# Kernel optimization log

Hardware: AMD Instinct MI355X
Metric: run time of the kernel (lower is better)

## Reference

```python
import jax, jax.numpy as jnp
import numpy as np

B, S, H, V = 256, 15, 512, 50257

def setup_inputs() -> dict:
    key = jax.random.key(0)
    ks = jax.random.split(key, 12)
    sc_h = 1.0 / np.sqrt(H)
    sc_in = 1.0 / np.sqrt(2 * H)
    return {
        "input_tokens": jax.random.randint(ks[0], (B, 1), 0, V),
        "hidden": jax.random.normal(ks[1], (1, B, H), jnp.float32),
        "encoder_outputs": jax.random.normal(ks[2], (B, S, H), jnp.float32),
        "emb_table": jax.random.normal(ks[3], (V, H), jnp.float32),
        "attn_W": jax.random.uniform(ks[4], (H, H), jnp.float32, -sc_h, sc_h),
        "attn_b": jax.random.uniform(ks[5], (H,), jnp.float32, -sc_h, sc_h),
        "W_ih": jax.random.uniform(ks[6], (3 * H, 2 * H), jnp.float32, -sc_in, sc_in),
        "W_hh": jax.random.uniform(ks[7], (3 * H, H), jnp.float32, -sc_h, sc_h),
        "b_ih": jax.random.uniform(ks[8], (3 * H,), jnp.float32, -sc_h, sc_h),
        "b_hh": jax.random.uniform(ks[9], (3 * H,), jnp.float32, -sc_h, sc_h),
        "out_W": jax.random.uniform(ks[10], (V, H), jnp.float32, -sc_h, sc_h),
        "out_b": jax.random.uniform(ks[11], (V,), jnp.float32, -sc_h, sc_h),
    }


def reference(input_tokens, hidden, encoder_outputs, emb_table, attn_W, attn_b,
              W_ih, W_hh, b_ih, b_hh, out_W, out_b):
    # Embedding (dropout is identity in eval/reference mode): [B,1,H]
    embedded = emb_table[input_tokens]
    h = hidden[0]  # [B,H]

    # Bahdanau-style scores, vectorized over the seq dim instead of the python loop:
    # energies[b,s] = attn(enc[b,s]);  score[b,s] = <h[b], energies[b,s]>
    energies = jnp.einsum("bsh,oh->bso", encoder_outputs, attn_W) + attn_b  # [B,S,H]
    attn_scores = jnp.einsum("bso,bo->bs", energies, h)                      # [B,S]
    attn_weights = jax.nn.softmax(attn_scores, axis=1)                       # [B,S]

    # context = weights @ encoder_outputs: [B,1,H]
    context = jnp.einsum("bs,bsh->bh", attn_weights, encoder_outputs)[:, None, :]

    # GRU single step (PyTorch gate order: r, z, n)
    x = jnp.concatenate([embedded, context], axis=2)[:, 0]  # [B,2H]
    gi = x @ W_ih.T + b_ih   # [B,3H]
    gh = h @ W_hh.T + b_hh   # [B,3H]
    i_r, i_z, i_n = jnp.split(gi, 3, axis=1)
    h_r, h_z, h_n = jnp.split(gh, 3, axis=1)
    r = jax.nn.sigmoid(i_r + h_r)
    z = jax.nn.sigmoid(i_z + h_z)
    n = jnp.tanh(i_n + r * h_n)
    h_new = (1.0 - z) * n + z * h            # [B,H]

    logits = h_new[:, None, :] @ out_W.T + out_b   # [B,1,V]
    log_probs = jax.nn.log_softmax(logits, axis=-1)
    return log_probs, h_new[None], attn_weights
```

## Files before the change

kernel.cpp:

```cpp
#include <hip/hip_runtime.h>

#define V_SIZE 50257
#define B_SIZE 256
#define S_LEN  15
#define H_DIM  512
#define NBLK_LG 1571

typedef __attribute__((ext_vector_type(8))) short bf16x8;
typedef __attribute__((ext_vector_type(4))) float f32x4;

__device__ __forceinline__ unsigned short f2bf(float f) {
    unsigned int u = __float_as_uint(f);
    u += 0x7fffu + ((u >> 16) & 1u);
    return (unsigned short)(u >> 16);
}

__global__ __launch_bounds__(256) void u_kernel(
    const float* __restrict__ hidden, const float* __restrict__ attn_W,
    float* __restrict__ u)
{
    __shared__ float h_s[16][H_DIM];
    const int tid = threadIdx.x;
    const int b0 = blockIdx.y * 16, n0 = blockIdx.x * 32;
    const float4* hv = (const float4*)(hidden + (size_t)b0 * H_DIM);
    float4* hs4 = (float4*)&h_s[0][0];
    #pragma unroll
    for (int i = 0; i < 8; ++i) hs4[tid + i * 256] = hv[tid + i * 256];
    __syncthreads();
    const int n = n0 + (tid & 31);
    const int m = (tid >> 5) * 2;
    float a0 = 0.f, a1 = 0.f;
    #pragma unroll 8
    for (int o = 0; o < H_DIM; ++o) {
        float w = attn_W[(size_t)o * H_DIM + n];
        a0 += h_s[m][o] * w;
        a1 += h_s[m + 1][o] * w;
    }
    u[(size_t)(b0 + m) * H_DIM + n] = a0;
    u[(size_t)(b0 + m + 1) * H_DIM + n] = a1;
}

__global__ __launch_bounds__(256) void attn_kernel(
    const float* __restrict__ hidden, const float* __restrict__ enc,
    const float* __restrict__ u, const int* __restrict__ tokens,
    const float* __restrict__ emb, float* __restrict__ attnw_out,
    unsigned short* __restrict__ x_bf, unsigned short* __restrict__ h_bf)
{
    const int b = blockIdx.x, tid = threadIdx.x;
    __shared__ float u_s[H_DIM];
    __shared__ float sc_s[S_LEN];
    __shared__ float w_s[S_LEN];
    u_s[tid]       = u[(size_t)b * H_DIM + tid];
    u_s[tid + 256] = u[(size_t)b * H_DIM + tid + 256];
    h_bf[(size_t)b * H_DIM + tid]       = f2bf(hidden[(size_t)b * H_DIM + tid]);
    h_bf[(size_t)b * H_DIM + tid + 256] = f2bf(hidden[(size_t)b * H_DIM + tid + 256]);
    const int tok = tokens[b];
    x_bf[(size_t)b * 2 * H_DIM + tid]       = f2bf(emb[(size_t)tok * H_DIM + tid]);
    x_bf[(size_t)b * 2 * H_DIM + tid + 256] = f2bf(emb[(size_t)tok * H_DIM + tid + 256]);
    __syncthreads();
    const int wave = tid >> 6, lane = tid & 63;
    for (int s = wave; s < S_LEN; s += 4) {
        const float* e = enc + ((size_t)b * S_LEN + s) * H_DIM;
        float acc = 0.f;
        #pragma unroll
        for (int k = 0; k < H_DIM / 64; ++k) acc += e[lane + k * 64] * u_s[lane + k * 64];
        #pragma unroll
        for (int off = 32; off; off >>= 1) acc += __shfl_down(acc, off);
        if (lane == 0) sc_s[s] = acc;
    }
    __syncthreads();
    float mx = -1e30f;
    for (int s = 0; s < S_LEN; ++s) mx = fmaxf(mx, sc_s[s]);
    float sum = 0.f;
    for (int s = 0; s < S_LEN; ++s) sum += __expf(sc_s[s] - mx);
    const float inv = 1.f / sum;
    if (tid < S_LEN) {
        float w = __expf(sc_s[tid] - mx) * inv;
        w_s[tid] = w;
        attnw_out[b * S_LEN + tid] = w;
    }
    __syncthreads();
    #pragma unroll
    for (int hh = 0; hh < 2; ++hh) {
        int h = tid + hh * 256;
        float c = 0.f;
        #pragma unroll
        for (int s = 0; s < S_LEN; ++s)
            c += w_s[s] * enc[((size_t)b * S_LEN + s) * H_DIM + h];
        x_bf[(size_t)b * 2 * H_DIM + H_DIM + h] = f2bf(c);
    }
}

struct GemmP {
    const unsigned short* A; const float* B; const float* bias; float* C;
    int N; int K;
};

template<int BM, int BN, int BK, int WR, int WC>
__global__ __launch_bounds__(256) void gemm_nt(GemmP p0, GemmP p1)
{
    GemmP p = (blockIdx.z == 0) ? p0 : p1;
    constexpr int LDA = BK + 8;
    __shared__ __align__(16) unsigned short As[BM][LDA];
    __shared__ __align__(16) unsigned short Bs[BN][LDA];
    const int tid = threadIdx.x;
    const int bn0 = blockIdx.x * BN;
    const int bm0 = blockIdx.y * BM;
    const int wave = tid >> 6, lane = tid & 63;
    const int wm = (wave / WC) * (BM / WR);
    const int wn = (wave % WC) * (BN / WC);
    constexpr int MF = BM / WR / 16, NF = BN / WC / 16;
    const int n16 = lane & 15, quad = lane >> 4;

    f32x4 acc[MF][NF] = {};

    for (int k0 = 0; k0 < p.K; k0 += BK) {
        #pragma unroll
        for (int it = 0; it < BM / 32; ++it) {
            int v = it * 256 + tid;
            int row = v >> 3, seg = v & 7;
            *(uint4*)&As[row][seg * 8] =
                *(const uint4*)(p.A + (size_t)(bm0 + row) * p.K + k0 + seg * 8);
        }
        #pragma unroll
        for (int it = 0; it < BN / 32; ++it) {
            int v = it * 256 + tid;
            int row = v >> 3, seg = v & 7;
            int gv = bn0 + row;
            float4 w0 = make_float4(0, 0, 0, 0), w1 = make_float4(0, 0, 0, 0);
            if (gv < p.N) {
                const float4* src = (const float4*)(p.B + (size_t)gv * p.K + k0 + seg * 8);
                w0 = src[0]; w1 = src[1];
            }
            uint4 pk;
            pk.x = (unsigned)f2bf(w0.x) | ((unsigned)f2bf(w0.y) << 16);
            pk.y = (unsigned)f2bf(w0.z) | ((unsigned)f2bf(w0.w) << 16);
            pk.z = (unsigned)f2bf(w1.x) | ((unsigned)f2bf(w1.y) << 16);
            pk.w = (unsigned)f2bf(w1.z) | ((unsigned)f2bf(w1.w) << 16);
            *(uint4*)&Bs[row][seg * 8] = pk;
        }
        __syncthreads();
        #pragma unroll
        for (int kk = 0; kk < BK; kk += 32) {
            bf16x8 af[MF], bfr[NF];
            #pragma unroll
            for (int i = 0; i < MF; ++i)
                af[i] = *(const bf16x8*)&As[wm + i * 16 + n16][kk + quad * 8];
            #pragma unroll
            for (int j = 0; j < NF; ++j)
                bfr[j] = *(const bf16x8*)&Bs[wn + j * 16 + n16][kk + quad * 8];
            #pragma unroll
            for (int i = 0; i < MF; ++i)
                #pragma unroll
                for (int j = 0; j < NF; ++j)
                    acc[i][j] = __builtin_amdgcn_mfma_f32_16x16x32_bf16(
                        af[i], bfr[j], acc[i][j], 0, 0, 0);
        }
        __syncthreads();
    }
    #pragma unroll
    for (int i = 0; i < MF; ++i) {
        const int r0 = bm0 + wm + i * 16 + quad * 4;
        #pragma unroll
        for (int j = 0; j < NF; ++j) {
            const int c = bn0 + wn + j * 16 + n16;
            if (c < p.N) {
                const float bv = p.bias[c];
                #pragma unroll
                for (int r = 0; r < 4; ++r)
                    p.C[(size_t)(r0 + r) * p.N + c] = acc[i][j][r] + bv;
            }
        }
    }
}

template<bool PART>
__global__ __launch_bounds__(256, 4) void gemm_lg(
    const unsigned short* __restrict__ A, const float* __restrict__ B,
    const float* __restrict__ bias, float* __restrict__ C,
    float* __restrict__ pm, float* __restrict__ ps)
{
    constexpr int BN = 32, BK = H_DIM;
    constexpr int LDB = BK + 8;
    __shared__ __align__(16) unsigned short Bs[BN][LDB];
    const int tid = threadIdx.x;
    const int bn0 = blockIdx.x * BN;
    const int wave = tid >> 6, lane = tid & 63;
    const int wm = wave * 64;
    const int n16 = lane & 15, quad = lane >> 4;

    {
        float4 w0[8], w1[8];
        #pragma unroll
        for (int it = 0; it < 8; ++it) {
            int v = it * 256 + tid;
            int row = v >> 6, seg = v & 63;
            int gv = bn0 + row;
            float4 z; z.x = z.y = z.z = z.w = 0.f;
            w0[it] = z; w1[it] = z;
            if (gv < V_SIZE) {
                const float4* src = (const float4*)(B + (size_t)gv * H_DIM + seg * 8);
                w0[it] = src[0]; w1[it] = src[1];
            }
        }
        #pragma unroll
        for (int it = 0; it < 8; ++it) {
            int v = it * 256 + tid;
            int row = v >> 6, seg = v & 63;
            uint4 pk;
            pk.x = (unsigned)f2bf(w0[it].x) | ((unsigned)f2bf(w0[it].y) << 16);
            pk.y = (unsigned)f2bf(w0[it].z) | ((unsigned)f2bf(w0[it].w) << 16);
            pk.z = (unsigned)f2bf(w1[it].x) | ((unsigned)f2bf(w1[it].y) << 16);
            pk.w = (unsigned)f2bf(w1[it].z) | ((unsigned)f2bf(w1[it].w) << 16);
            *(uint4*)&Bs[row][seg * 8] = pk;
        }
    }
    __syncthreads();

    f32x4 acc[4][2] = {};
    const unsigned short* arow[4];
    #pragma unroll
    for (int i = 0; i < 4; ++i)
        arow[i] = A + (size_t)(wm + i * 16 + n16) * H_DIM + quad * 8;

    bf16x8 af[4], afn[4];
    #pragma unroll
    for (int i = 0; i < 4; ++i) af[i] = *(const bf16x8*)(arow[i]);

    #pragma unroll
    for (int kk = 0; kk < BK; kk += 32) {
        if (kk + 32 < BK) {
            #pragma unroll
            for (int i = 0; i < 4; ++i)
                afn[i] = *(const bf16x8*)(arow[i] + kk + 32);
        }
        bf16x8 bfr[2];
        #pragma unroll
        for (int j = 0; j < 2; ++j)
            bfr[j] = *(const bf16x8*)&Bs[j * 16 + n16][kk + quad * 8];
        #pragma unroll
        for (int i = 0; i < 4; ++i)
            #pragma unroll
            for (int j = 0; j < 2; ++j)
                acc[i][j] = __builtin_amdgcn_mfma_f32_16x16x32_bf16(
                    af[i], bfr[j], acc[i][j], 0, 0, 0);
        #pragma unroll
        for (int i = 0; i < 4; ++i) af[i] = afn[i];
    }

    int cj[2]; float bvv[2]; bool okj[2];
    #pragma unroll
    for (int j = 0; j < 2; ++j) {
        cj[j] = bn0 + j * 16 + n16;
        okj[j] = cj[j] < V_SIZE;
        bvv[j] = okj[j] ? bias[cj[j]] : 0.f;
    }
    #pragma unroll
    for (int i = 0; i < 4; ++i) {
        const int r0 = wm + i * 16 + quad * 4;
        if (PART) {
            #pragma unroll
            for (int r = 0; r < 4; ++r) {
                float m = -1e30f;
                #pragma unroll
                for (int j = 0; j < 2; ++j)
                    if (okj[j]) m = fmaxf(m, acc[i][j][r] + bvv[j]);
                #pragma unroll
                for (int d = 1; d < 16; d <<= 1) m = fmaxf(m, __shfl_xor(m, d));
                float s = 0.f;
                #pragma unroll
                for (int j = 0; j < 2; ++j)
                    if (okj[j]) s += __expf(acc[i][j][r] + bvv[j] - m);
                #pragma unroll
                for (int d = 1; d < 16; d <<= 1) s += __shfl_xor(s, d);
                if (n16 == 0) {
                    pm[(size_t)blockIdx.x * B_SIZE + r0 + r] = m;
                    ps[(size_t)blockIdx.x * B_SIZE + r0 + r] = s;
                }
            }
        }
        #pragma unroll
        for (int j = 0; j < 2; ++j) if (okj[j]) {
            #pragma unroll
            for (int r = 0; r < 4; ++r)
                C[(size_t)(r0 + r) * V_SIZE + cj[j]] = acc[i][j][r] + bvv[j];
        }
    }
}

__global__ __launch_bounds__(256) void gru_kernel(
    const float* __restrict__ gi, const float* __restrict__ gh,
    const float* __restrict__ hidden, float* __restrict__ hnew_out,
    unsigned short* __restrict__ hnew_bf)
{
    const int idx = blockIdx.x * 256 + threadIdx.x;
    const int b = idx >> 9, h = idx & 511;
    const float* gib = gi + (size_t)b * 3 * H_DIM;
    const float* ghb = gh + (size_t)b * 3 * H_DIM;
    float r = 1.f / (1.f + __expf(-(gib[h] + ghb[h])));
    float z = 1.f / (1.f + __expf(-(gib[H_DIM + h] + ghb[H_DIM + h])));
    float n = gib[2 * H_DIM + h] + r * ghb[2 * H_DIM + h];
    n = 1.f - 2.f / (1.f + __expf(2.f * n));
    float hp = hidden[idx];
    float hn = (1.f - z) * n + z * hp;
    hnew_out[idx] = hn;
    hnew_bf[idx] = f2bf(hn);
}

__global__ __launch_bounds__(512) void finalize_kernel(
    float* __restrict__ logits, const float* __restrict__ pm,
    const float* __restrict__ ps)
{
    const int b = blockIdx.x, tid = threadIdx.x;
    float m = -1e30f, s = 0.f;
    for (int i = tid; i < NBLK_LG; i += 512) {
        float mm = pm[(size_t)i * B_SIZE + b], ss = ps[(size_t)i * B_SIZE + b];
        float nm = fmaxf(m, mm);
        s = s * __expf(m - nm) + ss * __expf(mm - nm);
        m = nm;
    }
    const int lane = tid & 63, wave = tid >> 6;
    #pragma unroll
    for (int off = 32; off; off >>= 1) {
        float m2 = __shfl_down(m, off), s2 = __shfl_down(s, off);
        float nm = fmaxf(m, m2);
        s = s * __expf(m - nm) + s2 * __expf(m2 - nm);
        m = nm;
    }
    __shared__ float msh[8], ssh[8], lse_sh;
    if (lane == 0) { msh[wave] = m; ssh[wave] = s; }
    __syncthreads();
    if (tid == 0) {
        float M = msh[0], S = ssh[0];
        for (int w = 1; w < 8; ++w) {
            float nm = fmaxf(M, msh[w]);
            S = S * __expf(M - nm) + ssh[w] * __expf(msh[w] - nm);
            M = nm;
        }
        lse_sh = M + logf(S);
    }
    __syncthreads();
    const float lse = lse_sh;
    constexpr int QTR = (V_SIZE + 3) / 4;
    const int start = blockIdx.y * QTR;
    const int end = min(V_SIZE, start + QTR);
    float* row = logits + (size_t)b * V_SIZE;
    for (int c = start + tid; c < end; c += 512) row[c] -= lse;
}

__global__ __launch_bounds__(1024) void logsoftmax_kernel(float* __restrict__ logits)
{
    const int b = blockIdx.x, tid = threadIdx.x;
    float* row = logits + (size_t)b * V_SIZE;
    float m = -1e30f, s = 0.f;
    for (int c = tid; c < V_SIZE; c += 1024) {
        float x = row[c];
        float nm = fmaxf(m, x);
        s = s * __expf(m - nm) + __expf(x - nm);
        m = nm;
    }
    const int lane = tid & 63, wave = tid >> 6;
    #pragma unroll
    for (int off = 32; off; off >>= 1) {
        float m2 = __shfl_down(m, off), s2 = __shfl_down(s, off);
        float nm = fmaxf(m, m2);
        s = s * __expf(m - nm) + s2 * __expf(m2 - nm);
        m = nm;
    }
    __shared__ float msh[16], ssh[16], lse_sh;
    if (lane == 0) { msh[wave] = m; ssh[wave] = s; }
    __syncthreads();
    if (tid == 0) {
        float M = msh[0], S = ssh[0];
        for (int w = 1; w < 16; ++w) {
            float nm = fmaxf(M, msh[w]);
            S = S * __expf(M - nm) + ssh[w] * __expf(msh[w] - nm);
            M = nm;
        }
        lse_sh = M + logf(S);
    }
    __syncthreads();
    const float lse = lse_sh;
    for (int c = tid; c < V_SIZE; c += 1024) row[c] -= lse;
}

constexpr size_t OFF_U      = 0;
constexpr size_t OFF_XBF    = 524288;
constexpr size_t OFF_HBF    = 1048576;
constexpr size_t OFF_HNEWBF = 1310720;
constexpr size_t OFF_GI     = 1572864;
constexpr size_t OFF_GH     = 3145728;
constexpr size_t OFF_PM     = 4718592;
constexpr size_t OFF_PS     = 6327296;
constexpr size_t WS_NEED    = 7936000;

extern "C" void kernel_launch(void* const* d_in, const int* in_sizes, int n_in,
                              void* d_out, int out_size, void* d_ws, size_t ws_size,
                              hipStream_t stream) {
    const int*   tokens = (const int*)d_in[0];
    const float* hidden = (const float*)d_in[1];
    const float* enc    = (const float*)d_in[2];
    const float* emb    = (const float*)d_in[3];
    const float* attn_W = (const float*)d_in[4];
    const float* W_ih   = (const float*)d_in[6];
    const float* W_hh   = (const float*)d_in[7];
    const float* b_ih   = (const float*)d_in[8];
    const float* b_hh   = (const float*)d_in[9];
    const float* out_W  = (const float*)d_in[10];
    const float* out_b  = (const float*)d_in[11];

    float* out = (float*)d_out;
    float* logp      = out;
    float* hnew_out  = out + (size_t)B_SIZE * V_SIZE;
    float* attnw_out = hnew_out + (size_t)B_SIZE * H_DIM;

    char* ws = (char*)d_ws;
    float*          u_ws    = (float*)(ws + OFF_U);
    unsigned short* x_bf    = (unsigned short*)(ws + OFF_XBF);
    unsigned short* h_bf    = (unsigned short*)(ws + OFF_HBF);
    unsigned short* hnew_bf = (unsigned short*)(ws + OFF_HNEWBF);
    float*          gi_ws   = (float*)(ws + OFF_GI);
    float*          gh_ws   = (float*)(ws + OFF_GH);
    float*          pm_ws   = (float*)(ws + OFF_PM);
    float*          ps_ws   = (float*)(ws + OFF_PS);

    u_kernel<<<dim3(16, 16), 256, 0, stream>>>(hidden, attn_W, u_ws);
    attn_kernel<<<dim3(256), 256, 0, stream>>>(hidden, enc, u_ws, tokens, emb,
                                               attnw_out, x_bf, h_bf);
    GemmP gi_p { x_bf, W_ih, b_ih, gi_ws, 3 * H_DIM, 2 * H_DIM };
    GemmP gh_p { h_bf, W_hh, b_hh, gh_ws, 3 * H_DIM, H_DIM };
    gemm_nt<64, 64, 64, 2, 2><<<dim3(24, 4, 2), 256, 0, stream>>>(gi_p, gh_p);
    gru_kernel<<<dim3(512), 256, 0, stream>>>(gi_ws, gh_ws, hidden, hnew_out, hnew_bf);

    if (ws_size >= WS_NEED) {
        gemm_lg<true><<<dim3(NBLK_LG), 256, 0, stream>>>(
            hnew_bf, out_W, out_b, logp, pm_ws, ps_ws);
        finalize_kernel<<<dim3(256, 4), 512, 0, stream>>>(logp, pm_ws, ps_ws);
    } else {
        gemm_lg<false><<<dim3(NBLK_LG), 256, 0, stream>>>(
            hnew_bf, out_W, out_b, logp, nullptr, nullptr);
        logsoftmax_kernel<<<dim3(256), 1024, 0, stream>>>(logp);
    }
}
```

Measured before the change: 403.3 us.

## Load output weights directly into MFMA registers and split log-softmax reduction

```diff
diff --git a/kernel.cpp b/kernel.cpp
--- a/kernel.cpp
+++ b/kernel.cpp
@@ -5,6 +5,7 @@
 #define S_LEN  15
 #define H_DIM  512
 #define NBLK_LG 1571
+#define NRED   32
 
 typedef __attribute__((ext_vector_type(8))) short bf16x8;
 typedef __attribute__((ext_vector_type(4))) float f32x4;
@@ -180,64 +181,58 @@
     const float* __restrict__ bias, float* __restrict__ C,
     float* __restrict__ pm, float* __restrict__ ps)
 {
-    constexpr int BN = 32, BK = H_DIM;
-    constexpr int LDB = BK + 8;
-    __shared__ __align__(16) unsigned short Bs[BN][LDB];
     const int tid = threadIdx.x;
-    const int bn0 = blockIdx.x * BN;
+    const int bn0 = blockIdx.x * 32;
     const int wave = tid >> 6, lane = tid & 63;
     const int wm = wave * 64;
     const int n16 = lane & 15, quad = lane >> 4;
 
-    {
-        float4 w0[8], w1[8];
-        #pragma unroll
-        for (int it = 0; it < 8; ++it) {
-            int v = it * 256 + tid;
-            int row = v >> 6, seg = v & 63;
-            int gv = bn0 + row;
-            float4 z; z.x = z.y = z.z = z.w = 0.f;
-            w0[it] = z; w1[it] = z;
-            if (gv < V_SIZE) {
-                const float4* src = (const float4*)(B + (size_t)gv * H_DIM + seg * 8);
-                w0[it] = src[0]; w1[it] = src[1];
-            }
-        }
-        #pragma unroll
-        for (int it = 0; it < 8; ++it) {
-            int v = it * 256 + tid;
-            int row = v >> 6, seg = v & 63;
-            uint4 pk;
-            pk.x = (unsigned)f2bf(w0[it].x) | ((unsigned)f2bf(w0[it].y) << 16);
-            pk.y = (unsigned)f2bf(w0[it].z) | ((unsigned)f2bf(w0[it].w) << 16);
-            pk.z = (unsigned)f2bf(w1[it].x) | ((unsigned)f2bf(w1[it].y) << 16);
-            pk.w = (unsigned)f2bf(w1[it].z) | ((unsigned)f2bf(w1[it].w) << 16);
-            *(uint4*)&Bs[row][seg * 8] = pk;
-        }
-    }
-    __syncthreads();
-
-    f32x4 acc[4][2] = {};
     const unsigned short* arow[4];
     #pragma unroll
     for (int i = 0; i < 4; ++i)
         arow[i] = A + (size_t)(wm + i * 16 + n16) * H_DIM + quad * 8;
-
-    bf16x8 af[4], afn[4];
+    const float* brow[2];
+    #pragma unroll
+    for (int j = 0; j < 2; ++j) {
+        int r = bn0 + j * 16 + n16;
+        if (r >= V_SIZE) r = V_SIZE - 1;
+        brow[j] = B + (size_t)r * H_DIM + quad * 8;
+    }
+
+    f32x4 acc[4][2] = {};
+    bf16x8 af[4];
+    float4 bw0[2], bw1[2];
     #pragma unroll
     for (int i = 0; i < 4; ++i) af[i] = *(const bf16x8*)(arow[i]);
-
-    #pragma unroll
-    for (int kk = 0; kk < BK; kk += 32) {
-        if (kk + 32 < BK) {
+    #pragma unroll
+    for (int j = 0; j < 2; ++j) {
+        bw0[j] = *(const float4*)(brow[j]);
+        bw1[j] = *(const float4*)(brow[j] + 4);
+    }
+
+    #pragma unroll
+    for (int kk = 0; kk < H_DIM; kk += 32) {
+        bf16x8 afn[4]; float4 nw0[2], nw1[2];
+        if (kk + 32 < H_DIM) {
             #pragma unroll
             for (int i = 0; i < 4; ++i)
                 afn[i] = *(const bf16x8*)(arow[i] + kk + 32);
+            #pragma unroll
+            for (int j = 0; j < 2; ++j) {
+                nw0[j] = *(const float4*)(brow[j] + kk + 32);
+                nw1[j] = *(const float4*)(brow[j] + kk + 32 + 4);
+            }
         }
         bf16x8 bfr[2];
         #pragma unroll
-        for (int j = 0; j < 2; ++j)
-            bfr[j] = *(const bf16x8*)&Bs[j * 16 + n16][kk + quad * 8];
+        for (int j = 0; j < 2; ++j) {
+            bf16x8 t;
+            t[0] = (short)f2bf(bw0[j].x); t[1] = (short)f2bf(bw0[j].y);
+            t[2] = (short)f2bf(bw0[j].z); t[3] = (short)f2bf(bw0[j].w);
+            t[4] = (short)f2bf(bw1[j].x); t[5] = (short)f2bf(bw1[j].y);
+            t[6] = (short)f2bf(bw1[j].z); t[7] = (short)f2bf(bw1[j].w);
+            bfr[j] = t;
+        }
         #pragma unroll
         for (int i = 0; i < 4; ++i)
             #pragma unroll
@@ -246,6 +241,8 @@
                     af[i], bfr[j], acc[i][j], 0, 0, 0);
         #pragma unroll
         for (int i = 0; i < 4; ++i) af[i] = afn[i];
+        #pragma unroll
+        for (int j = 0; j < 2; ++j) { bw0[j] = nw0[j]; bw1[j] = nw1[j]; }
     }
 
     int cj[2]; float bvv[2]; bool okj[2];
@@ -307,40 +304,39 @@
     hnew_bf[idx] = f2bf(hn);
 }
 
-__global__ __launch_bounds__(512) void finalize_kernel(
-    float* __restrict__ logits, const float* __restrict__ pm,
-    const float* __restrict__ ps)
-{
-    const int b = blockIdx.x, tid = threadIdx.x;
+__global__ __launch_bounds__(256) void reduce1_kernel(
+    const float* __restrict__ pm, const float* __restrict__ ps,
+    float* __restrict__ pm2, float* __restrict__ ps2)
+{
+    const int b = threadIdx.x;
+    constexpr int CHUNK = (NBLK_LG + NRED - 1) / NRED;
+    const int i0 = blockIdx.x * CHUNK;
+    const int i1 = min(NBLK_LG, i0 + CHUNK);
     float m = -1e30f, s = 0.f;
-    for (int i = tid; i < NBLK_LG; i += 512) {
+    for (int i = i0; i < i1; ++i) {
         float mm = pm[(size_t)i * B_SIZE + b], ss = ps[(size_t)i * B_SIZE + b];
         float nm = fmaxf(m, mm);
         s = s * __expf(m - nm) + ss * __expf(mm - nm);
         m = nm;
     }
-    const int lane = tid & 63, wave = tid >> 6;
-    #pragma unroll
-    for (int off = 32; off; off >>= 1) {
-        float m2 = __shfl_down(m, off), s2 = __shfl_down(s, off);
-        float nm = fmaxf(m, m2);
-        s = s * __expf(m - nm) + s2 * __expf(m2 - nm);
+    pm2[(size_t)blockIdx.x * B_SIZE + b] = m;
+    ps2[(size_t)blockIdx.x * B_SIZE + b] = s;
+}
+
+__global__ __launch_bounds__(512) void finalize_kernel(
+    float* __restrict__ logits, const float* __restrict__ pm2,
+    const float* __restrict__ ps2)
+{
+    const int b = blockIdx.x, tid = threadIdx.x;
+    float m = -1e30f, s = 0.f;
+    #pragma unroll
+    for (int j = 0; j < NRED; ++j) {
+        float mm = pm2[(size_t)j * B_SIZE + b], ss = ps2[(size_t)j * B_SIZE + b];
+        float nm = fmaxf(m, mm);
+        s = s * __expf(m - nm) + ss * __expf(mm - nm);
         m = nm;
     }
-    __shared__ float msh[8], ssh[8], lse_sh;
-    if (lane == 0) { msh[wave] = m; ssh[wave] = s; }
-    __syncthreads();
-    if (tid == 0) {
-        float M = msh[0], S = ssh[0];
-        for (int w = 1; w < 8; ++w) {
-            float nm = fmaxf(M, msh[w]);
-            S = S * __expf(M - nm) + ssh[w] * __expf(msh[w] - nm);
-            M = nm;
-        }
-        lse_sh = M + logf(S);
-    }
-    __syncthreads();
-    const float lse = lse_sh;
+    const float lse = m + logf(s);
     constexpr int QTR = (V_SIZE + 3) / 4;
     const int start = blockIdx.y * QTR;
     const int end = min(V_SIZE, start + QTR);
@@ -392,7 +388,9 @@
 constexpr size_t OFF_GH     = 3145728;
 constexpr size_t OFF_PM     = 4718592;
 constexpr size_t OFF_PS     = 6327296;
-constexpr size_t WS_NEED    = 7936000;
+constexpr size_t OFF_PM2    = 7936000;
+constexpr size_t OFF_PS2    = 7968768;
+constexpr size_t WS_NEED    = 8001536;
 
 extern "C" void kernel_launch(void* const* d_in, const int* in_sizes, int n_in,
                               void* d_out, int out_size, void* d_ws, size_t ws_size,
@@ -423,6 +421,8 @@
     float*          gh_ws   = (float*)(ws + OFF_GH);
     float*          pm_ws   = (float*)(ws + OFF_PM);
     float*          ps_ws   = (float*)(ws + OFF_PS);
+    float*          pm2_ws  = (float*)(ws + OFF_PM2);
+    float*          ps2_ws  = (float*)(ws + OFF_PS2);
 
     u_kernel<<<dim3(16, 16), 256, 0, stream>>>(hidden, attn_W, u_ws);
     attn_kernel<<<dim3(256), 256, 0, stream>>>(hidden, enc, u_ws, tokens, emb,
@@ -435,7 +435,8 @@
     if (ws_size >= WS_NEED) {
         gemm_lg<true><<<dim3(NBLK_LG), 256, 0, stream>>>(
             hnew_bf, out_W, out_b, logp, pm_ws, ps_ws);
-        finalize_kernel<<<dim3(256, 4), 512, 0, stream>>>(logp, pm_ws, ps_ws);
+        reduce1_kernel<<<dim3(NRED), 256, 0, stream>>>(pm_ws, ps_ws, pm2_ws, ps2_ws);
+        finalize_kernel<<<dim3(256, 4), 512, 0, stream>>>(logp, pm2_ws, ps2_ws);
     } else {
         gemm_lg<false><<<dim3(NBLK_LG), 256, 0, stream>>>(
             hnew_bf, out_W, out_b, logp, nullptr, nullptr);
```

After: 438.5 us. +8.7%, slower.
